# Performance work log

Hardware: AMD Instinct MI355X
Metric: run time of the kernel (lower is better)

The kernel has to match this reference:

```python
import jax, jax.numpy as jnp
import numpy as np

D_MODEL = 1024
NUM_HEADS = 16
HEAD_DIM = D_MODEL // NUM_HEADS
ALPHA = 1.0


def setup_inputs() -> dict:
    key = jax.random.key(0)
    ks = jax.random.split(key, 9)
    B, T, D = 2, 2048, D_MODEL
    s = 1.0 / np.sqrt(D)
    inp = {
        "x": jax.random.normal(ks[0], (B, T, D), dtype=jnp.float32),
        "Wq": jax.random.uniform(ks[1], (D, D), jnp.float32, -s, s),
        "bq": jax.random.uniform(ks[2], (D,), jnp.float32, -s, s),
        "Wk": jax.random.uniform(ks[3], (D, D), jnp.float32, -s, s),
        "bk": jax.random.uniform(ks[4], (D,), jnp.float32, -s, s),
        "Wv": jax.random.uniform(ks[5], (D, D), jnp.float32, -s, s),
        "bv": jax.random.uniform(ks[6], (D,), jnp.float32, -s, s),
        "Wo": jax.random.uniform(ks[7], (D, D), jnp.float32, -s, s),
        "bo": jax.random.uniform(ks[8], (D,), jnp.float32, -s, s),
    }
    return inp


def reference(x, Wq, bq, Wk, bk, Wv, bv, Wo, bo):
    B, T, D = x.shape
    H, hd = NUM_HEADS, HEAD_DIM

    def split_heads(y):  # [B,T,D] -> [B,H,T,hd]
        return y.reshape(B, T, H, hd).transpose(0, 2, 1, 3)

    Q = split_heads(x @ Wq.T + bq)
    K = split_heads(x @ Wk.T + bk)
    V = split_heads(x @ Wv.T + bv)

    scores = jnp.einsum('bhid,bhjd->bhij', Q, K) / jnp.sqrt(jnp.float32(hd))

    t = jnp.arange(T)
    delta = t[:, None] - t[None, :]  # [T,T], i - j
    causal_mask = delta < 0          # j > i (strict upper triangle)
    # similarity_power_law decay bias: -(delta)^alpha for delta >= 0, else 0
    decay = jnp.where(causal_mask, 0.0, -(delta.astype(jnp.float32) ** ALPHA))

    scores = jnp.where(causal_mask, -jnp.inf, scores) + decay
    attn = jax.nn.softmax(scores, axis=-1)

    out = jnp.einsum('bhij,bhjd->bhid', attn, V)
    out = out.transpose(0, 2, 1, 3).reshape(B, T, D)
    return out @ Wo.T + bo
```

## Files before the change

### kernel.cpp

```cpp
#include <hip/hip_runtime.h>

#define TT 2048
#define DD 1024
#define HH 16
#define HD 64
#define NTOK 4096

typedef __bf16 bf16x8 __attribute__((ext_vector_type(8)));
typedef short short4v __attribute__((ext_vector_type(4)));
typedef float f32x4 __attribute__((ext_vector_type(4)));

__device__ __forceinline__ unsigned short f2bf(float f) {
  unsigned u = __float_as_uint(f);
  u += 0x7fffu + ((u >> 16) & 1u);
  return (unsigned short)(u >> 16);
}

#if __has_builtin(__builtin_amdgcn_mfma_f32_16x16x16bf16_1k)
__device__ __forceinline__ f32x4 mfma16(short4v a, short4v b, f32x4 c) {
  return __builtin_amdgcn_mfma_f32_16x16x16bf16_1k(a, b, c, 0, 0, 0);
}
#else
__device__ __forceinline__ f32x4 mfma16(short4v a, short4v b, f32x4 c) {
  asm("v_mfma_f32_16x16x16_bf16 %0, %1, %2, %0\n\ts_nop 7\n\ts_nop 7"
      : "+v"(c) : "v"(a), "v"(b));
  return c;
}
#endif

typedef void __attribute__((address_space(1))) as1_void;
typedef void __attribute__((address_space(3))) as3_void;
__device__ __forceinline__ void gl_lds16(const void* g, void* l) {
  __builtin_amdgcn_global_load_lds((as1_void*)g, (as3_void*)l, 16, 0, 0);
}

__global__ __launch_bounds__(256)
void wcmha_cast_all(const float4* __restrict__ x,  const float4* __restrict__ wq,
                    const float4* __restrict__ wk, const float4* __restrict__ wv,
                    const float4* __restrict__ wo,
                    ushort4* __restrict__ xb,  ushort4* __restrict__ wqb,
                    ushort4* __restrict__ wkb, ushort4* __restrict__ wvb,
                    ushort4* __restrict__ wob) {
  const int i = blockIdx.x * 256 + threadIdx.x;
  const float4* src;
  ushort4* dst;
  int off;
  if (i < 1048576) {
    src = x; dst = xb; off = i;
  } else {
    int j = i - 1048576;
    int sel = j >> 18;
    off = j & 262143;
    const float4* ws_[4] = {wq, wk, wv, wo};
    ushort4* wd_[4] = {wqb, wkb, wvb, wob};
    src = ws_[sel]; dst = wd_[sel];
  }
  float4 v = src[off];
  ushort4 o;
  o.x = f2bf(v.x); o.y = f2bf(v.y); o.z = f2bf(v.z); o.w = f2bf(v.w);
  dst[off] = o;
}

template <int BN_, bool SWAP>
__device__ __forceinline__ void gemm_db(const unsigned short* __restrict__ X,
                                        const unsigned short* __restrict__ W,
                                        int m0, int n0,
                                        unsigned short* As, unsigned short* Bs,
                                        f32x4 acc[4][BN_ / 32]) {
  constexpr int NI = BN_ / 32;
  constexpr int JB = (BN_ * 4) / 256;
  const int tid = threadIdx.x, wid = tid >> 6, lane = tid & 63;
  const int m = lane & 15, quad = lane >> 4;
  const int wm = (wid >> 1) * 64, wn = (wid & 1) * (BN_ / 2);
  const int xq = (quad ^ ((m >> 1) & 3)) * 8;

  const unsigned short* gA[2];
  const unsigned short* gB[JB];
#pragma unroll
  for (int j = 0; j < 2; ++j) {
    int c = wid * 64 + lane + j * 256;
    gA[j] = X + (size_t)(m0 + (c >> 2)) * DD + ((c & 3) ^ ((c >> 3) & 3)) * 8;
  }
#pragma unroll
  for (int j = 0; j < JB; ++j) {
    int c = wid * 64 + lane + j * 256;
    gB[j] = W + (size_t)(n0 + (c >> 2)) * DD + ((c & 3) ^ ((c >> 3) & 3)) * 8;
  }
  unsigned short* lA[2][2];
  unsigned short* lB[2][JB];
#pragma unroll
  for (int p = 0; p < 2; ++p) {
#pragma unroll
    for (int j = 0; j < 2; ++j)
      lA[p][j] = As + p * (128 * 32) + (wid * 64 + j * 256) * 8;
#pragma unroll
    for (int j = 0; j < JB; ++j)
      lB[p][j] = Bs + p * (BN_ * 32) + (wid * 64 + j * 256) * 8;
  }

#pragma unroll
  for (int i = 0; i < 4; ++i)
#pragma unroll
    for (int j = 0; j < NI; ++j) acc[i][j] = (f32x4){0.f, 0.f, 0.f, 0.f};

#pragma unroll
  for (int j = 0; j < 2; ++j) gl_lds16(gA[j], lA[0][j]);
#pragma unroll
  for (int j = 0; j < JB; ++j) gl_lds16(gB[j], lB[0][j]);

  for (int k = 0; k < 32; ++k) {
    const int p = k & 1;
    __syncthreads();
    if (k < 31) {
      const int k1 = (k + 1) * 32;
#pragma unroll
      for (int j = 0; j < 2; ++j) gl_lds16(gA[j] + k1, lA[p ^ 1][j]);
#pragma unroll
      for (int j = 0; j < JB; ++j) gl_lds16(gB[j] + k1, lB[p ^ 1][j]);
    }
    const unsigned short* ap = As + p * (128 * 32);
    const unsigned short* bp = Bs + p * (BN_ * 32);
    bf16x8 af[4], bf[NI];
#pragma unroll
    for (int mi = 0; mi < 4; ++mi)
      af[mi] = *(const bf16x8*)&ap[(wm + mi * 16 + m) * 32 + xq];
#pragma unroll
    for (int ni = 0; ni < NI; ++ni)
      bf[ni] = *(const bf16x8*)&bp[(wn + ni * 16 + m) * 32 + xq];
#pragma unroll
    for (int mi = 0; mi < 4; ++mi)
#pragma unroll
      for (int ni = 0; ni < NI; ++ni)
        acc[mi][ni] = SWAP
            ? __builtin_amdgcn_mfma_f32_16x16x32_bf16(bf[ni], af[mi], acc[mi][ni], 0, 0, 0)
            : __builtin_amdgcn_mfma_f32_16x16x32_bf16(af[mi], bf[ni], acc[mi][ni], 0, 0, 0);
  }
}

__global__ __launch_bounds__(256)
void wcmha_gemm_qkv(const unsigned short* __restrict__ X,
                    const unsigned short* __restrict__ Wq,
                    const unsigned short* __restrict__ Wk,
                    const unsigned short* __restrict__ Wv,
                    const float* __restrict__ bq, const float* __restrict__ bk,
                    const float* __restrict__ bv,
                    unsigned short* __restrict__ Qb,
                    unsigned short* __restrict__ Kb,
                    unsigned short* __restrict__ Vt) {
  __shared__ unsigned short As[2 * 128 * 32];
  __shared__ unsigned short Bs[2 * 128 * 32];
  const int mat = blockIdx.y >> 3;
  const int m0 = blockIdx.x * 128;
  const int n0 = (blockIdx.y & 7) * 128;

  const int lane = threadIdx.x & 63, wid = threadIdx.x >> 6;
  const int m = lane & 15, quad = lane >> 4;
  const int wm = (wid >> 1) * 64, wn = (wid & 1) * 64;

  f32x4 acc[4][4];
  if (mat < 2) {
    const unsigned short* W = mat ? Wk : Wq;
    const float* bias = mat ? bk : bq;
    unsigned short* dst = mat ? Kb : Qb;
    gemm_db<128, false>(X, W, m0, n0, As, Bs, acc);
#pragma unroll
    for (int mi = 0; mi < 4; ++mi)
#pragma unroll
      for (int ni = 0; ni < 4; ++ni) {
        int col = n0 + wn + ni * 16 + m;
        int h = col >> 6, d = col & 63;
        float bb = bias[col];
#pragma unroll
        for (int r = 0; r < 4; ++r) {
          int row = m0 + wm + mi * 16 + quad * 4 + r;
          int b = row >> 11, t = row & (TT - 1);
          dst[((size_t)(b * HH + h) * TT + t) * HD + d] = f2bf(acc[mi][ni][r] + bb);
        }
      }
  } else {
    gemm_db<128, true>(X, Wv, m0, n0, As, Bs, acc);
#pragma unroll
    for (int mi = 0; mi < 4; ++mi) {
      int row = m0 + wm + mi * 16 + m;
      int b = row >> 11, t = row & (TT - 1);
#pragma unroll
      for (int ni = 0; ni < 4; ++ni)
#pragma unroll
        for (int r = 0; r < 4; ++r) {
          int col = n0 + wn + ni * 16 + quad * 4 + r;
          int h = col >> 6, d = col & 63;
          Vt[((size_t)(b * HH + h) * HD + d) * TT + t] = f2bf(acc[mi][ni][r] + bv[col]);
        }
    }
  }
}

__global__ __launch_bounds__(256)
void wcmha_gemm_out(const unsigned short* __restrict__ X,
                    const unsigned short* __restrict__ W,
                    const float* __restrict__ bias,
                    float* __restrict__ Y) {
  __shared__ unsigned short As[2 * 128 * 32];
  __shared__ unsigned short Bs[2 * 64 * 32];
  const int m0 = blockIdx.x * 128;
  const int n0 = blockIdx.y * 64;
  const int lane = threadIdx.x & 63, wid = threadIdx.x >> 6;
  const int m = lane & 15, quad = lane >> 4;
  const int wm = (wid >> 1) * 64, wn = (wid & 1) * 32;

  f32x4 acc[4][2];
  gemm_db<64, false>(X, W, m0, n0, As, Bs, acc);

#pragma unroll
  for (int mi = 0; mi < 4; ++mi)
#pragma unroll
    for (int ni = 0; ni < 2; ++ni) {
      int col = n0 + wn + ni * 16 + m;
      float bb = bias[col];
#pragma unroll
      for (int r = 0; r < 4; ++r) {
        int row = m0 + wm + mi * 16 + quad * 4 + r;
        Y[(size_t)row * DD + col] = acc[mi][ni][r] + bb;
      }
    }
}

__global__ __launch_bounds__(256)
void wcmha_attn(const unsigned short* __restrict__ Qb,
                const unsigned short* __restrict__ Kb,
                const unsigned short* __restrict__ Vt,
                unsigned short* __restrict__ O) {
  const int wid = threadIdx.x >> 6, lane = threadIdx.x & 63;
  const int gw = (blockIdx.x << 2) + wid;
  const int qt = gw & 127, bh = gw >> 7;
  const int qbase = qt << 4;
  const int il = lane & 15, quad = lane >> 4;
  const int ig = qbase + il;

  const unsigned short* q_ptr = Qb + (size_t)bh * TT * HD;
  const unsigned short* k_ptr = Kb + (size_t)bh * TT * HD;
  const unsigned short* v_ptr = Vt + (size_t)bh * HD * TT;

  const bf16x8 qf0 = *(const bf16x8*)(q_ptr + (size_t)ig * HD + quad * 8);
  const bf16x8 qf1 = *(const bf16x8*)(q_ptr + (size_t)ig * HD + 32 + quad * 8);

  const int j0 = (qbase >= 48) ? qbase - 48 : 0;

  f32x4 st[4];
#pragma unroll
  for (int jt = 0; jt < 4; ++jt) {
    const unsigned short* kp = k_ptr + (size_t)(j0 + jt * 16 + il) * HD;
    bf16x8 k0 = *(const bf16x8*)(kp + quad * 8);
    bf16x8 k1 = *(const bf16x8*)(kp + 32 + quad * 8);
    f32x4 a = {0.f, 0.f, 0.f, 0.f};
    a = __builtin_amdgcn_mfma_f32_16x16x32_bf16(k0, qf0, a, 0, 0, 0);
    a = __builtin_amdgcn_mfma_f32_16x16x32_bf16(k1, qf1, a, 0, 0, 0);
    st[jt] = a;
  }

  float mloc = -3.0e38f;
#pragma unroll
  for (int jt = 0; jt < 4; ++jt)
#pragma unroll
    for (int r = 0; r < 4; ++r) {
      int jg = j0 + jt * 16 + quad * 4 + r;
      float v = (jg > ig) ? -3.0e38f : st[jt][r] * 0.125f - (float)(ig - jg);
      st[jt][r] = v;
      mloc = fmaxf(mloc, v);
    }
  mloc = fmaxf(mloc, __shfl_xor(mloc, 16));
  mloc = fmaxf(mloc, __shfl_xor(mloc, 32));

  float rs = 0.f;
  short4v pf[4];
#pragma unroll
  for (int jt = 0; jt < 4; ++jt)
#pragma unroll
    for (int r = 0; r < 4; ++r) {
      float p = __expf(st[jt][r] - mloc);
      rs += p;
      pf[jt][r] = (short)f2bf(p);
    }
  rs += __shfl_xor(rs, 16);
  rs += __shfl_xor(rs, 32);

  f32x4 o_acc[4];
#pragma unroll
  for (int nt = 0; nt < 4; ++nt) o_acc[nt] = (f32x4){0.f, 0.f, 0.f, 0.f};
#pragma unroll
  for (int jt = 0; jt < 4; ++jt)
#pragma unroll
    for (int nt = 0; nt < 4; ++nt) {
      short4v vf = *(const short4v*)(v_ptr + (size_t)(nt * 16 + il) * TT +
                                     j0 + jt * 16 + quad * 4);
      o_acc[nt] = mfma16(vf, pf[jt], o_acc[nt]);
    }

  const float inv_l = 1.f / rs;
  const int b = bh >> 4, hh = bh & 15;
  unsigned short* ob = O + ((size_t)(b * TT + ig)) * DD + hh * HD;
#pragma unroll
  for (int nt = 0; nt < 4; ++nt)
#pragma unroll
    for (int r = 0; r < 4; ++r)
      ob[nt * 16 + quad * 4 + r] = f2bf(o_acc[nt][r] * inv_l);
}

extern "C" void kernel_launch(void* const* d_in, const int* in_sizes, int n_in,
                              void* d_out, int out_size, void* d_ws, size_t ws_size,
                              hipStream_t stream) {
  const float* x  = (const float*)d_in[0];
  const float* Wq = (const float*)d_in[1];
  const float* bq = (const float*)d_in[2];
  const float* Wk = (const float*)d_in[3];
  const float* bk = (const float*)d_in[4];
  const float* Wv = (const float*)d_in[5];
  const float* bv = (const float*)d_in[6];
  const float* Wo = (const float*)d_in[7];
  const float* bo = (const float*)d_in[8];

  char* ws = (char*)d_ws;
  unsigned short* xb  = (unsigned short*)(ws);
  unsigned short* wqb = (unsigned short*)(ws + (8u << 20));
  unsigned short* wkb = wqb + (1u << 20);
  unsigned short* wvb = wkb + (1u << 20);
  unsigned short* wob = wvb + (1u << 20);
  unsigned short* Qb  = (unsigned short*)(ws + (16u << 20));
  unsigned short* Kb  = (unsigned short*)(ws + (24u << 20));
  unsigned short* Vt  = (unsigned short*)(ws + (32u << 20));
  unsigned short* Ob  = xb;

  wcmha_cast_all<<<8192, 256, 0, stream>>>(
      (const float4*)x, (const float4*)Wq, (const float4*)Wk,
      (const float4*)Wv, (const float4*)Wo,
      (ushort4*)xb, (ushort4*)wqb, (ushort4*)wkb, (ushort4*)wvb, (ushort4*)wob);

  wcmha_gemm_qkv<<<dim3(32, 24), 256, 0, stream>>>(xb, wqb, wkb, wvb,
                                                   bq, bk, bv, Qb, Kb, Vt);

  wcmha_attn<<<1024, 256, 0, stream>>>(Qb, Kb, Vt, Ob);

  wcmha_gemm_out<<<dim3(32, 16), 256, 0, stream>>>(Ob, wob, bo, (float*)d_out);
}
```

Measured before the change: 167.8 us.

## Triple-buffer GEMM LDS tiles with explicit vmcnt waits and prefetch depth two

Replaces the double-buffered K loop in the projection GEMMs with a three-stage ring of LDS buffers. Loads now run two k-steps ahead, and partial s_waitcnt vmcnt waits plus a raw s_barrier stand in for __syncthreads. The aim is to hide more global-to-LDS latency behind MFMA work. In exchange it uses 1.5x the LDS, which may reduce occupancy, and it relies on the hand-computed vmcnt counts being correct.

```diff
diff --git a/kernel.cpp b/kernel.cpp
--- a/kernel.cpp
+++ b/kernel.cpp
@@ -62,13 +62,14 @@
 }
 
 template <int BN_, bool SWAP>
-__device__ __forceinline__ void gemm_db(const unsigned short* __restrict__ X,
+__device__ __forceinline__ void gemm_p3(const unsigned short* __restrict__ X,
                                         const unsigned short* __restrict__ W,
                                         int m0, int n0,
                                         unsigned short* As, unsigned short* Bs,
                                         f32x4 acc[4][BN_ / 32]) {
   constexpr int NI = BN_ / 32;
   constexpr int JB = (BN_ * 4) / 256;
+  constexpr int NL = 2 + JB;
   const int tid = threadIdx.x, wid = tid >> 6, lane = tid & 63;
   const int m = lane & 15, quad = lane >> 4;
   const int wm = (wid >> 1) * 64, wn = (wid & 1) * (BN_ / 2);
@@ -86,10 +87,10 @@
     int c = wid * 64 + lane + j * 256;
     gB[j] = W + (size_t)(n0 + (c >> 2)) * DD + ((c & 3) ^ ((c >> 3) & 3)) * 8;
   }
-  unsigned short* lA[2][2];
-  unsigned short* lB[2][JB];
-#pragma unroll
-  for (int p = 0; p < 2; ++p) {
+  unsigned short* lA[3][2];
+  unsigned short* lB[3][JB];
+#pragma unroll
+  for (int p = 0; p < 3; ++p) {
 #pragma unroll
     for (int j = 0; j < 2; ++j)
       lA[p][j] = As + p * (128 * 32) + (wid * 64 + j * 256) * 8;
@@ -104,19 +105,33 @@
     for (int j = 0; j < NI; ++j) acc[i][j] = (f32x4){0.f, 0.f, 0.f, 0.f};
 
 #pragma unroll
-  for (int j = 0; j < 2; ++j) gl_lds16(gA[j], lA[0][j]);
-#pragma unroll
-  for (int j = 0; j < JB; ++j) gl_lds16(gB[j], lB[0][j]);
+  for (int kk = 0; kk < 2; ++kk) {
+    const int ko = kk * 32;
+#pragma unroll
+    for (int j = 0; j < 2; ++j) gl_lds16(gA[j] + ko, lA[kk][j]);
+#pragma unroll
+    for (int j = 0; j < JB; ++j) gl_lds16(gB[j] + ko, lB[kk][j]);
+  }
 
   for (int k = 0; k < 32; ++k) {
-    const int p = k & 1;
-    __syncthreads();
+    const int p = k - (k / 3) * 3;
     if (k < 31) {
-      const int k1 = (k + 1) * 32;
-#pragma unroll
-      for (int j = 0; j < 2; ++j) gl_lds16(gA[j] + k1, lA[p ^ 1][j]);
-#pragma unroll
-      for (int j = 0; j < JB; ++j) gl_lds16(gB[j] + k1, lB[p ^ 1][j]);
+      if constexpr (NL == 4)
+        asm volatile("s_waitcnt vmcnt(4)" ::: "memory");
+      else
+        asm volatile("s_waitcnt vmcnt(3)" ::: "memory");
+    } else {
+      asm volatile("s_waitcnt vmcnt(0)" ::: "memory");
+    }
+    __builtin_amdgcn_s_barrier();
+    if (k + 2 < 32) {
+      const int kq = k + 2;
+      const int b = kq - (kq / 3) * 3;
+      const int ko = kq * 32;
+#pragma unroll
+      for (int j = 0; j < 2; ++j) gl_lds16(gA[j] + ko, lA[b][j]);
+#pragma unroll
+      for (int j = 0; j < JB; ++j) gl_lds16(gB[j] + ko, lB[b][j]);
     }
     const unsigned short* ap = As + p * (128 * 32);
     const unsigned short* bp = Bs + p * (BN_ * 32);
@@ -147,8 +162,8 @@
                     unsigned short* __restrict__ Qb,
                     unsigned short* __restrict__ Kb,
                     unsigned short* __restrict__ Vt) {
-  __shared__ unsigned short As[2 * 128 * 32];
-  __shared__ unsigned short Bs[2 * 128 * 32];
+  __shared__ unsigned short As[3 * 128 * 32];
+  __shared__ unsigned short Bs[3 * 128 * 32];
   const int mat = blockIdx.y >> 3;
   const int m0 = blockIdx.x * 128;
   const int n0 = (blockIdx.y & 7) * 128;
@@ -162,7 +177,7 @@
     const unsigned short* W = mat ? Wk : Wq;
     const float* bias = mat ? bk : bq;
     unsigned short* dst = mat ? Kb : Qb;
-    gemm_db<128, false>(X, W, m0, n0, As, Bs, acc);
+    gemm_p3<128, false>(X, W, m0, n0, As, Bs, acc);
 #pragma unroll
     for (int mi = 0; mi < 4; ++mi)
 #pragma unroll
@@ -178,7 +193,7 @@
         }
       }
   } else {
-    gemm_db<128, true>(X, Wv, m0, n0, As, Bs, acc);
+    gemm_p3<128, true>(X, Wv, m0, n0, As, Bs, acc);
 #pragma unroll
     for (int mi = 0; mi < 4; ++mi) {
       int row = m0 + wm + mi * 16 + m;
@@ -200,8 +215,8 @@
                     const unsigned short* __restrict__ W,
                     const float* __restrict__ bias,
                     float* __restrict__ Y) {
-  __shared__ unsigned short As[2 * 128 * 32];
-  __shared__ unsigned short Bs[2 * 64 * 32];
+  __shared__ unsigned short As[3 * 128 * 32];
+  __shared__ unsigned short Bs[3 * 64 * 32];
   const int m0 = blockIdx.x * 128;
   const int n0 = blockIdx.y * 64;
   const int lane = threadIdx.x & 63, wid = threadIdx.x >> 6;
@@ -209,7 +224,7 @@
   const int wm = (wid >> 1) * 64, wn = (wid & 1) * 32;
 
   f32x4 acc[4][2];
-  gemm_db<64, false>(X, W, m0, n0, As, Bs, acc);
+  gemm_p3<64, false>(X, W, m0, n0, As, Bs, acc);
 
 #pragma unroll
   for (int mi = 0; mi < 4; ++mi)
```

New measurement: 171.4 us. 2.1% more time.
